# Kernel optimization log

Measured on AMD Instinct MI355X. Metric: run time of the kernel, lower is better.

## Reference

```python
import jax, jax.numpy as jnp
import numpy as np

N_QUBITS = 4
INV_SQRT2 = np.float32(1.0 / np.sqrt(2.0))
CNOT_PAIRS = [(0, 1), (1, 2), (2, 3), (3, 0), (0, 2), (1, 3), (2, 0), (3, 1)]


def _apply_1q(state, U, w):
    # state: (B,2,2,2,2); U: (B,2,2) batched or (2,2) shared
    state = jnp.moveaxis(state, w + 1, 1)
    if U.ndim == 3:
        state = jnp.einsum('bij,bj...->bi...', U, state)
    else:
        state = jnp.einsum('ij,bj...->bi...', U, state)
    return jnp.moveaxis(state, 1, w + 1)


def _apply_cnot(state, c, t):
    st = jnp.moveaxis(state, (c + 1, t + 1), (1, 2))
    st = jnp.stack([st[:, 0], st[:, 1, ::-1]], axis=1)  # flip target where ctrl=1
    return jnp.moveaxis(st, (1, 2), (c + 1, t + 1))


def _ry_batched(theta):  # theta: (B,) -> (B,2,2) complex
    c, s = jnp.cos(theta * 0.5), jnp.sin(theta * 0.5)
    return jnp.stack([jnp.stack([c, -s], -1), jnp.stack([s, c], -1)], -2).astype(jnp.complex64)


def _rz_batched(theta):  # theta: (B,) -> (B,2,2) complex (diag(e^{-i t/2}, e^{i t/2}))
    e = jnp.exp(-0.5j * theta.astype(jnp.complex64))
    z = jnp.zeros_like(e)
    return jnp.stack([jnp.stack([e, z], -1), jnp.stack([z, jnp.conj(e)], -1)], -2)


def _ry1(t):  # scalar -> (2,2)
    c, s = jnp.cos(t * 0.5), jnp.sin(t * 0.5)
    return jnp.stack([jnp.stack([c, -s]), jnp.stack([s, c])]).astype(jnp.complex64)


def _rz1(t):  # scalar -> (2,2)
    e = jnp.exp(-0.5j * t.astype(jnp.complex64))
    z = jnp.zeros_like(e)
    return jnp.stack([jnp.stack([e, z]), jnp.stack([z, jnp.conj(e)])])


def _circuit(f, weights):
    # f: (B, 4) angle features; weights: (L, 4, 3). Returns <Z_i> per wire: (B, 4).
    B = f.shape[0]
    state = jnp.zeros((B, 2, 2, 2, 2), jnp.complex64).at[:, 0, 0, 0, 0].set(1.0)
    H = jnp.array([[1.0, 1.0], [1.0, -1.0]], jnp.complex64) * INV_SQRT2
    for i in range(N_QUBITS):
        state = _apply_1q(state, H, i)
        state = _apply_1q(state, _ry_batched(jnp.arctan(f[:, i])), i)
        state = _apply_1q(state, _rz_batched(jnp.arctan(f[:, i] ** 2)), i)
    n_layers = weights.shape[0]
    for l in range(n_layers):
        for c, t in CNOT_PAIRS:
            state = _apply_cnot(state, c, t)
        for i in range(N_QUBITS):
            phi, theta, omega = weights[l, i, 0], weights[l, i, 1], weights[l, i, 2]
            # PennyLane Rot(phi, theta, omega) = RZ(omega) @ RY(theta) @ RZ(phi)
            U = _rz1(omega) @ _ry1(theta) @ _rz1(phi)
            state = _apply_1q(state, U, i)
    probs = jnp.abs(state) ** 2  # (B,2,2,2,2)
    z = []
    for i in range(N_QUBITS):
        axes = tuple(a for a in range(1, N_QUBITS + 1) if a != i + 1)
        m = probs.sum(axes)  # (B,2)
        z.append(m[:, 0] - m[:, 1])
    return jnp.stack(z, -1)


def setup_inputs() -> dict:
    key = jax.random.key(0)
    ks = jax.random.split(key, 6)
    B, D_IN, D_OUT, L = 131072, 256, 64, 2
    x = jax.random.normal(ks[0], (B, D_IN), jnp.float32)
    W1 = jax.random.normal(ks[1], (N_QUBITS, D_IN), jnp.float32) * (1.0 / np.sqrt(D_IN))
    b1 = jax.random.normal(ks[2], (N_QUBITS,), jnp.float32) * 0.1
    weights = jax.random.normal(ks[3], (L, N_QUBITS, 3), jnp.float32)
    W2 = jax.random.normal(ks[4], (D_OUT, N_QUBITS), jnp.float32) * 0.5
    b2 = jax.random.normal(ks[5], (D_OUT,), jnp.float32) * 0.1
    return {"x": x, "W1": W1, "b1": b1, "weights": weights, "W2": W2, "b2": b2}


def reference(x, W1, b1, weights, W2, b2):
    f = jnp.tanh(x @ W1.T + b1) * jnp.pi  # (B,4)
    q = _circuit(f, weights)              # (B,4) expval(PauliZ)
    return q @ W2.T + b2                  # (B, D_OUT)
```

## Files before the change

kernel.cpp:

```cpp
#include <hip/hip_runtime.h>
#include <math.h>

#define NQ 4
#define DIN 256
#define DOUT 64
#define NLAYER 2
#define TPB 256
#define BROWS 128
#define NIT (BROWS/8)
#define PF 3

__device__ __forceinline__ float tanh_fast(float y) {
    float e = __expf(2.0f * y);
    return 1.0f - 2.0f / (e + 1.0f);
}

__global__ __launch_bounds__(TPB, 4) void qp_fused(
    const float* __restrict__ x,  const float* __restrict__ W1,
    const float* __restrict__ b1, const float* __restrict__ wts,
    const float* __restrict__ W2, const float* __restrict__ b2,
    float* __restrict__ out)
{
    __shared__ __align__(16) float fs[BROWS][NQ];
    __shared__ __align__(16) float qs[BROWS][NQ];
    __shared__ __align__(16) float w2s[DOUT][NQ];
    __shared__ __align__(16) float us[8][8];
    __shared__ float b2s[DOUT];

    const int t = threadIdx.x;
    const int wave = t >> 6, lane = t & 63;
    const int half = lane >> 5;
    const int cl   = lane & 31;
    const int brow = blockIdx.x * BROWS;

    if (t < 64) {
        ((float4*)&w2s[0][0])[t] = ((const float4*)W2)[t];
        b2s[t] = b2[t];
    }
    if (t < 8) {
        const float phi = wts[t*3 + 0], th = wts[t*3 + 1], om = wts[t*3 + 2];
        float sth, cth; sincosf(0.5f*th, &sth, &cth);
        float sp, cp;   sincosf(0.5f*(phi+om), &sp, &cp);
        float sm, cm;   sincosf(0.5f*(phi-om), &sm, &cm);
        us[t][0] =  cth*cp; us[t][1] = -cth*sp;
        us[t][2] = -sth*cm; us[t][3] = -sth*sm;
        us[t][4] =  sth*cm; us[t][5] = -sth*sm;
        us[t][6] =  cth*cp; us[t][7] =  cth*sp;
    }

    {
        float4 w[4][2];
        #pragma unroll
        for (int q = 0; q < 4; ++q) {
            w[q][0] = ((const float4*)W1)[q*64 + cl];
            w[q][1] = ((const float4*)W1)[q*64 + 32 + cl];
        }
        const float4 bv = *(const float4*)b1;
        const int qsel = lane & 3;
        const float bsel = (qsel==0)?bv.x:(qsel==1)?bv.y:(qsel==2)?bv.z:bv.w;

        const int row0 = brow + wave*2 + half;

        float4 buf[PF+1][2];
        #pragma unroll
        for (int k = 0; k < PF; ++k) {
            const float4* xn = (const float4*)(x + (size_t)(row0 + k*8) * DIN);
            buf[k][0] = xn[cl]; buf[k][1] = xn[32 + cl];
        }

        #pragma unroll
        for (int it = 0; it < NIT; ++it) {
            if (it + PF < NIT) {
                const float4* xn = (const float4*)(x + (size_t)(row0 + (it+PF)*8) * DIN);
                buf[(it+PF)&PF][0] = xn[cl];
                buf[(it+PF)&PF][1] = xn[32 + cl];
            }
            const float4 xv0 = buf[it&PF][0];
            const float4 xv1 = buf[it&PF][1];

            float a0, a1, a2, a3;
            a0 = fmaf(xv0.x,w[0][0].x, fmaf(xv0.y,w[0][0].y, fmaf(xv0.z,w[0][0].z, xv0.w*w[0][0].w)));
            a1 = fmaf(xv0.x,w[1][0].x, fmaf(xv0.y,w[1][0].y, fmaf(xv0.z,w[1][0].z, xv0.w*w[1][0].w)));
            a2 = fmaf(xv0.x,w[2][0].x, fmaf(xv0.y,w[2][0].y, fmaf(xv0.z,w[2][0].z, xv0.w*w[2][0].w)));
            a3 = fmaf(xv0.x,w[3][0].x, fmaf(xv0.y,w[3][0].y, fmaf(xv0.z,w[3][0].z, xv0.w*w[3][0].w)));
            a0 = fmaf(xv1.x,w[0][1].x, fmaf(xv1.y,w[0][1].y, fmaf(xv1.z,w[0][1].z, fmaf(xv1.w,w[0][1].w, a0))));
            a1 = fmaf(xv1.x,w[1][1].x, fmaf(xv1.y,w[1][1].y, fmaf(xv1.z,w[1][1].z, fmaf(xv1.w,w[1][1].w, a1))));
            a2 = fmaf(xv1.x,w[2][1].x, fmaf(xv1.y,w[2][1].y, fmaf(xv1.z,w[2][1].z, fmaf(xv1.w,w[2][1].w, a2))));
            a3 = fmaf(xv1.x,w[3][1].x, fmaf(xv1.y,w[3][1].y, fmaf(xv1.z,w[3][1].z, fmaf(xv1.w,w[3][1].w, a3))));

            a0 += __shfl_xor(a0, 1, 64);  a1 += __shfl_xor(a1, 1, 64);
            a2 += __shfl_xor(a2, 1, 64);  a3 += __shfl_xor(a3, 1, 64);
            a0 += __shfl_xor(a0, 2, 64);  a1 += __shfl_xor(a1, 2, 64);
            a2 += __shfl_xor(a2, 2, 64);  a3 += __shfl_xor(a3, 2, 64);
            float v = (qsel==0)?a0:(qsel==1)?a1:(qsel==2)?a2:a3;
            v += __shfl_xor(v, 4, 64);
            v += __shfl_xor(v, 8, 64);
            v += __shfl_xor(v, 16, 64);

            if (cl < 4) {
                const float PI = 3.14159265358979f;
                fs[it*8 + wave*2 + half][qsel] = PI * tanh_fast(v + bsel);
            }
        }
    }
    __syncthreads();

    if (t < BROWS) {
        const float4 fv = ((const float4*)fs)[t];
        const float fq[4] = {fv.x, fv.y, fv.z, fv.w};
        const float IS2 = 0.70710678118654752f;
        float vr[4][2], vi[4][2];
        #pragma unroll
        for (int i = 0; i < 4; ++i) {
            const float fi = fq[i];
            const float f2 = fi*fi;
            const float ca = rsqrtf(1.0f + f2);
            const float ch = sqrtf(0.5f*(1.0f + ca));
            const float sh = copysignf(sqrtf(fmaxf(0.5f*(1.0f - ca), 0.0f)), fi);
            const float cb = rsqrtf(1.0f + f2*f2);
            const float cbh = sqrtf(0.5f*(1.0f + cb));
            const float sbh = sqrtf(fmaxf(0.5f*(1.0f - cb), 0.0f));
            const float u0 = (ch - sh) * IS2;
            const float u1 = (ch + sh) * IS2;
            vr[i][0] = u0 * cbh;  vi[i][0] = -u0 * sbh;
            vr[i][1] = u1 * cbh;  vi[i][1] =  u1 * sbh;
        }
        float ar[16], ai[16];
        #pragma unroll
        for (int i0 = 0; i0 < 2; ++i0)
        #pragma unroll
        for (int i1 = 0; i1 < 2; ++i1) {
            const float pr  = vr[0][i0]*vr[1][i1] - vi[0][i0]*vi[1][i1];
            const float pim = vr[0][i0]*vi[1][i1] + vi[0][i0]*vr[1][i1];
            #pragma unroll
            for (int i2 = 0; i2 < 2; ++i2)
            #pragma unroll
            for (int i3 = 0; i3 < 2; ++i3) {
                const float qr  = vr[2][i2]*vr[3][i3] - vi[2][i2]*vi[3][i3];
                const float qim = vr[2][i2]*vi[3][i3] + vi[2][i2]*vr[3][i3];
                const int idx = i0*8 + i1*4 + i2*2 + i3;
                ar[idx] = pr*qr - pim*qim;
                ai[idx] = pr*qim + pim*qr;
            }
        }
        #pragma unroll
        for (int l = 0; l < NLAYER; ++l) {
            constexpr int cpairs[8][2] = {{0,1},{1,2},{2,3},{3,0},{0,2},{1,3},{2,0},{3,1}};
            #pragma unroll
            for (int g = 0; g < 8; ++g) {
                const int bc = 8 >> cpairs[g][0];
                const int bt = 8 >> cpairs[g][1];
                #pragma unroll
                for (int m = 0; m < 16; ++m) {
                    if ((m & bc) && !(m & bt)) {
                        const int m2 = m | bt;
                        float tr = ar[m]; ar[m] = ar[m2]; ar[m2] = tr;
                        float ti = ai[m]; ai[m] = ai[m2]; ai[m2] = ti;
                    }
                }
            }
            #pragma unroll
            for (int i = 0; i < 4; ++i) {
                const float* u = &us[l*4 + i][0];
                const float u00r=u[0], u00i=u[1], u01r=u[2], u01i=u[3];
                const float u10r=u[4], u10i=u[5], u11r=u[6], u11i=u[7];
                const int bq = 8 >> i;
                #pragma unroll
                for (int m = 0; m < 16; ++m) {
                    if (!(m & bq)) {
                        const int m2 = m | bq;
                        const float a0r=ar[m], a0i=ai[m], a1r=ar[m2], a1i=ai[m2];
                        ar[m]  = u00r*a0r - u00i*a0i + u01r*a1r - u01i*a1i;
                        ai[m]  = u00r*a0i + u00i*a0r + u01r*a1i + u01i*a1r;
                        ar[m2] = u10r*a0r - u10i*a0i + u11r*a1r - u11i*a1i;
                        ai[m2] = u10r*a0i + u10i*a0r + u11r*a1i + u11i*a1r;
                    }
                }
            }
        }
        float z0=0.f, z1=0.f, z2=0.f, z3=0.f;
        #pragma unroll
        for (int m = 0; m < 16; ++m) {
            const float p = ar[m]*ar[m] + ai[m]*ai[m];
            z0 += (m & 8) ? -p : p;
            z1 += (m & 4) ? -p : p;
            z2 += (m & 2) ? -p : p;
            z3 += (m & 1) ? -p : p;
        }
        float4 qv; qv.x=z0; qv.y=z1; qv.z=z2; qv.w=z3;
        ((float4*)qs)[t] = qv;
    }
    __syncthreads();

    {
        const int j4 = t & 15;
        const int rb = t >> 4;
        float w2r[4][4], b2r[4];
        #pragma unroll
        for (int jj = 0; jj < 4; ++jj) {
            const int j = j4*4 + jj;
            #pragma unroll
            for (int i = 0; i < 4; ++i) w2r[jj][i] = w2s[j][i];
            b2r[jj] = b2s[j];
        }
        #pragma unroll
        for (int e = 0; e < BROWS/16; ++e) {
            const int r = rb*(BROWS/16) + e;
            const float4 q = ((const float4*)qs)[r];
            float4 o;
            o.x = fmaf(q.x,w2r[0][0], fmaf(q.y,w2r[0][1], fmaf(q.z,w2r[0][2], fmaf(q.w,w2r[0][3], b2r[0]))));
            o.y = fmaf(q.x,w2r[1][0], fmaf(q.y,w2r[1][1], fmaf(q.z,w2r[1][2], fmaf(q.w,w2r[1][3], b2r[1]))));
            o.z = fmaf(q.x,w2r[2][0], fmaf(q.y,w2r[2][1], fmaf(q.z,w2r[2][2], fmaf(q.w,w2r[2][3], b2r[2]))));
            o.w = fmaf(q.x,w2r[3][0], fmaf(q.y,w2r[3][1], fmaf(q.z,w2r[3][2], fmaf(q.w,w2r[3][3], b2r[3]))));
            ((float4*)(out + (size_t)(brow + r) * DOUT))[j4] = o;
        }
    }
}

extern "C" void kernel_launch(void* const* d_in, const int* in_sizes, int n_in,
                              void* d_out, int out_size, void* d_ws, size_t ws_size,
                              hipStream_t stream) {
    const float* x  = (const float*)d_in[0];
    const float* W1 = (const float*)d_in[1];
    const float* b1 = (const float*)d_in[2];
    const float* wt = (const float*)d_in[3];
    const float* W2 = (const float*)d_in[4];
    const float* b2 = (const float*)d_in[5];
    float* out = (float*)d_out;
    const int B = in_sizes[0] / DIN;
    qp_fused<<<B / BROWS, TPB, 0, stream>>>(x, W1, b1, wt, W2, b2, out);
}
```

Measured before the change: 40.54 us.

## Make each wave own its rows end-to-end, dropping block-wide barriers

Each wave now handles 64 contiguous rows on its own. It does the projection, runs the circuit on all 64 lanes (previously only 128 threads of 256 did), and does the output projection, using per-wave shared slices. This removes the two block-level __syncthreads between stages and lets waves in a block overlap different phases. It also idles fewer lanes in the circuit stage. The grid halves, launch bounds drop to 2 blocks per CU, and within a wave the shared-memory handoff between lanes now relies on implicit wave-level synchronisation.

Result: faster. 38.81 us (-4.3%).

```diff
diff --git a/kernel.cpp b/kernel.cpp
--- a/kernel.cpp
+++ b/kernel.cpp
@@ -6,8 +6,8 @@
 #define DOUT 64
 #define NLAYER 2
 #define TPB 256
-#define BROWS 128
-#define NIT (BROWS/8)
+#define WROWS 64
+#define NIT (WROWS/2)
 #define PF 3
 
 __device__ __forceinline__ float tanh_fast(float y) {
@@ -15,14 +15,14 @@
     return 1.0f - 2.0f / (e + 1.0f);
 }
 
-__global__ __launch_bounds__(TPB, 4) void qp_fused(
+__global__ __launch_bounds__(TPB, 2) void qp_fused(
     const float* __restrict__ x,  const float* __restrict__ W1,
     const float* __restrict__ b1, const float* __restrict__ wts,
     const float* __restrict__ W2, const float* __restrict__ b2,
     float* __restrict__ out)
 {
-    __shared__ __align__(16) float fs[BROWS][NQ];
-    __shared__ __align__(16) float qs[BROWS][NQ];
+    __shared__ __align__(16) float fs[4][WROWS][NQ];
+    __shared__ __align__(16) float qs[4][WROWS][NQ];
     __shared__ __align__(16) float w2s[DOUT][NQ];
     __shared__ __align__(16) float us[8][8];
     __shared__ float b2s[DOUT];
@@ -31,7 +31,7 @@
     const int wave = t >> 6, lane = t & 63;
     const int half = lane >> 5;
     const int cl   = lane & 31;
-    const int brow = blockIdx.x * BROWS;
+    const int qsel = lane & 3;
 
     if (t < 64) {
         ((float4*)&w2s[0][0])[t] = ((const float4*)W2)[t];
@@ -47,6 +47,11 @@
         us[t][4] =  sth*cm; us[t][5] = -sth*sm;
         us[t][6] =  cth*cp; us[t][7] =  cth*sp;
     }
+    __syncthreads();
+
+    const int wrow = (blockIdx.x * 4 + wave) * WROWS;
+    float (* __restrict__ fsw)[NQ] = fs[wave];
+    float (* __restrict__ qsw)[NQ] = qs[wave];
 
     {
         float4 w[4][2];
@@ -56,22 +61,21 @@
             w[q][1] = ((const float4*)W1)[q*64 + 32 + cl];
         }
         const float4 bv = *(const float4*)b1;
-        const int qsel = lane & 3;
         const float bsel = (qsel==0)?bv.x:(qsel==1)?bv.y:(qsel==2)?bv.z:bv.w;
 
-        const int row0 = brow + wave*2 + half;
+        const int row0 = wrow + half;
 
         float4 buf[PF+1][2];
         #pragma unroll
         for (int k = 0; k < PF; ++k) {
-            const float4* xn = (const float4*)(x + (size_t)(row0 + k*8) * DIN);
+            const float4* xn = (const float4*)(x + (size_t)(row0 + k*2) * DIN);
             buf[k][0] = xn[cl]; buf[k][1] = xn[32 + cl];
         }
 
         #pragma unroll
         for (int it = 0; it < NIT; ++it) {
             if (it + PF < NIT) {
-                const float4* xn = (const float4*)(x + (size_t)(row0 + (it+PF)*8) * DIN);
+                const float4* xn = (const float4*)(x + (size_t)(row0 + (it+PF)*2) * DIN);
                 buf[(it+PF)&PF][0] = xn[cl];
                 buf[(it+PF)&PF][1] = xn[32 + cl];
             }
@@ -99,14 +103,13 @@
 
             if (cl < 4) {
                 const float PI = 3.14159265358979f;
-                fs[it*8 + wave*2 + half][qsel] = PI * tanh_fast(v + bsel);
-            }
-        }
-    }
-    __syncthreads();
-
-    if (t < BROWS) {
-        const float4 fv = ((const float4*)fs)[t];
+                fsw[it*2 + half][qsel] = PI * tanh_fast(v + bsel);
+            }
+        }
+    }
+
+    {
+        const float4 fv = *(const float4*)fsw[lane];
         const float fq[4] = {fv.x, fv.y, fv.z, fv.w};
         const float IS2 = 0.70710678118654752f;
         float vr[4][2], vi[4][2];
@@ -188,13 +191,12 @@
             z3 += (m & 1) ? -p : p;
         }
         float4 qv; qv.x=z0; qv.y=z1; qv.z=z2; qv.w=z3;
-        ((float4*)qs)[t] = qv;
-    }
-    __syncthreads();
+        *(float4*)qsw[lane] = qv;
+    }
 
     {
-        const int j4 = t & 15;
-        const int rb = t >> 4;
+        const int j4 = lane & 15;
+        const int rb = lane >> 4;
         float w2r[4][4], b2r[4];
         #pragma unroll
         for (int jj = 0; jj < 4; ++jj) {
@@ -204,15 +206,15 @@
             b2r[jj] = b2s[j];
         }
         #pragma unroll
-        for (int e = 0; e < BROWS/16; ++e) {
-            const int r = rb*(BROWS/16) + e;
-            const float4 q = ((const float4*)qs)[r];
+        for (int e = 0; e < WROWS/4; ++e) {
+            const int r = e*4 + rb;
+            const float4 q = *(const float4*)qsw[r];
             float4 o;
             o.x = fmaf(q.x,w2r[0][0], fmaf(q.y,w2r[0][1], fmaf(q.z,w2r[0][2], fmaf(q.w,w2r[0][3], b2r[0]))));
             o.y = fmaf(q.x,w2r[1][0], fmaf(q.y,w2r[1][1], fmaf(q.z,w2r[1][2], fmaf(q.w,w2r[1][3], b2r[1]))));
             o.z = fmaf(q.x,w2r[2][0], fmaf(q.y,w2r[2][1], fmaf(q.z,w2r[2][2], fmaf(q.w,w2r[2][3], b2r[2]))));
             o.w = fmaf(q.x,w2r[3][0], fmaf(q.y,w2r[3][1], fmaf(q.z,w2r[3][2], fmaf(q.w,w2r[3][3], b2r[3]))));
-            ((float4*)(out + (size_t)(brow + r) * DOUT))[j4] = o;
+            ((float4*)(out + (size_t)(wrow + r) * DOUT))[j4] = o;
         }
     }
 }
@@ -228,5 +230,5 @@
     const float* b2 = (const float*)d_in[5];
     float* out = (float*)d_out;
     const int B = in_sizes[0] / DIN;
-    qp_fused<<<B / BROWS, TPB, 0, stream>>>(x, W1, b1, wt, W2, b2, out);
+    qp_fused<<<B / (WROWS * 4), TPB, 0, stream>>>(x, W1, b1, wt, W2, b2, out);
 }
```
